# Performance work log

Measured on AMD Instinct MI355X. Metric: run time of the kernel, lower is better.

Reference implementation:

```python
import math
import jax, jax.numpy as jnp
import numpy as np

B, T, E, H = 4, 2048, 1024, 16
S = E // H
SCALE = 1.0 / math.sqrt(S)
LN_EPS = 1e-5


def setup_inputs() -> dict:
    key = jax.random.key(0)
    ks = jax.random.split(key, 5)
    w_std = 1.0 / math.sqrt(E)
    return {
        "x": jax.random.normal(ks[0], (B, T, E), jnp.float32),
        "Wq": jax.random.normal(ks[1], (E, E), jnp.float32) * w_std,
        "Wk": jax.random.normal(ks[2], (E, E), jnp.float32) * w_std,
        "Wv": jax.random.normal(ks[3], (E, E), jnp.float32) * w_std,
        "Wu": jax.random.normal(ks[4], (E, E), jnp.float32) * w_std,
        "bu": jnp.zeros((E,), jnp.float32),
        "q_gamma": jnp.ones((S,), jnp.float32),
        "q_beta": jnp.zeros((S,), jnp.float32),
        "k_gamma": jnp.ones((S,), jnp.float32),
        "k_beta": jnp.zeros((S,), jnp.float32),
    }


def _layernorm(x, gamma, beta):
    # normalize over last (head) dim, eps matches torch LayerNorm default
    mu = jnp.mean(x, axis=-1, keepdims=True)
    var = jnp.mean(jnp.square(x - mu), axis=-1, keepdims=True)
    return (x - mu) * jax.lax.rsqrt(var + LN_EPS) * gamma + beta


def reference(x, Wq, Wk, Wv, Wu, bu, q_gamma, q_beta, k_gamma, k_beta):
    b, t, e = x.shape
    h, s = H, S
    # torch Linear: y = x @ W^T ; split into heads [b, t, h, s]
    q = (x @ Wq.T).reshape(b, t, h, s)
    k = (x @ Wk.T).reshape(b, t, h, s)
    v = (x @ Wv.T).reshape(b, t, h, s)
    # kqnorm: LayerNorm over head dim s
    q = _layernorm(q, q_gamma, q_beta)
    k = _layernorm(k, k_gamma, k_beta)
    # scaled dot-product scores [b, h, t, t]
    dots = jnp.einsum("bthd,bThd->bhtT", q, k) * SCALE
    causal = jnp.tril(jnp.ones((t, t), dtype=bool))
    dots = jnp.where(causal, dots, jnp.finfo(dots.dtype).min)
    attn = jax.nn.softmax(dots, axis=-1)
    out = jnp.einsum("bhtT,bThd->bthd", attn, v).reshape(b, t, e)
    return out @ Wu.T + bu
```

## Files before the change

kernel.cpp:

```cpp
#include <hip/hip_runtime.h>
#include <hip/hip_bf16.h>
#include <stdint.h>
#include <stddef.h>


using bf16 = __hip_bfloat16;
typedef __attribute__((ext_vector_type(8))) short s16x8;
typedef __attribute__((ext_vector_type(4))) short s16x4;
typedef __attribute__((ext_vector_type(4))) float f32x4;

#define MFMA16(a, b, c) __builtin_amdgcn_mfma_f32_16x16x32_bf16((a), (b), (c), 0, 0, 0)

static __device__ __forceinline__ s16x8 ld8(const bf16* p) {
    return *reinterpret_cast<const s16x8*>(p);
}
static __device__ __forceinline__ s16x8 ld8s(const short* p) {
    return *reinterpret_cast<const s16x8*>(p);
}
static __device__ __forceinline__ s16x8 cvt8(const float* p) {
    f32x4 u = *reinterpret_cast<const f32x4*>(p);
    f32x4 v = *reinterpret_cast<const f32x4*>(p + 4);
    s16x8 r;
#pragma unroll
    for (int e = 0; e < 4; e++) {
        r[e]     = __builtin_bit_cast(short, __float2bfloat16(u[e]));
        r[e + 4] = __builtin_bit_cast(short, __float2bfloat16(v[e]));
    }
    return r;
}

static __device__ __forceinline__ void async16(short* lds, const bf16* g) {
    __builtin_amdgcn_global_load_lds(
        (const __attribute__((address_space(1))) unsigned int*)g,
        (__attribute__((address_space(3))) unsigned int*)lds, 16, 0, 0);
}

#define EE 1024

__global__ __launch_bounds__(256) void cvt_all(
    const float* __restrict__ w0, const float* __restrict__ w1,
    const float* __restrict__ w2, const float* __restrict__ w3,
    const float* __restrict__ x,
    bf16* __restrict__ o0, bf16* __restrict__ o1,
    bf16* __restrict__ o2, bf16* __restrict__ o3, bf16* __restrict__ xb)
{
    const int z = blockIdx.z;
    const float* s;
    bf16* d;
    if (z < 4) {
        s = (z == 0) ? w0 : (z == 1) ? w1 : (z == 2) ? w2 : w3;
        d = (z == 0) ? o0 : (z == 1) ? o1 : (z == 2) ? o2 : o3;
    } else {
        s = x  + (size_t)(z - 4) * 1048576;
        d = xb + (size_t)(z - 4) * 1048576;
    }
    size_t i = ((size_t)blockIdx.x * 256 + threadIdx.x) * 8;
    *reinterpret_cast<s16x8*>(d + i) = cvt8(s + i);
}

template <int AF32>
__global__ __launch_bounds__(256) void gemm_qkv_t(
    const float* __restrict__ xf, const bf16* __restrict__ xb,
    const bf16* __restrict__ Wq, const bf16* __restrict__ Wk, const bf16* __restrict__ Wv,
    bf16* __restrict__ Qb, bf16* __restrict__ Kb, bf16* __restrict__ Vb,
    const float* __restrict__ qg, const float* __restrict__ qbt,
    const float* __restrict__ kg, const float* __restrict__ kbt)
{
    constexpr int SA = AF32 ? 40 : 32;
    const int z = blockIdx.z;
    const bf16* Bt = (z == 0) ? Wq : (z == 1) ? Wk : Wv;
    bf16* out      = (z == 0) ? Qb : (z == 1) ? Kb : Vb;
    const float* gamma = (z == 0) ? qg : kg;
    const float* beta  = (z == 0) ? qbt : kbt;
    const bool  ln     = (z < 2);
    const float oscale = (z == 0) ? 0.125f : 1.0f;

    __shared__ __align__(16) short lA[128 * SA];
    __shared__ __align__(16) short lB[128 * 32];

    const int tid  = threadIdx.x;
    const int lane = tid & 63;
    const int w    = tid >> 6;
    const int wr = w >> 1, wc = w & 1;
    const int lr = lane & 15, quad = lane >> 4;

    const int m0 = blockIdx.y * 128;
    const int n0 = blockIdx.x * 128;

    const int strow = w * 32 + (lane >> 2);
    const int stcol = (lane & 3) * 8;
    const bf16* bgl = Bt + (size_t)(n0 + strow) * EE + stcol;
    short* bl = lB + (w * 2) * 512;

    const bf16* agl = nullptr;
    const float* ap = nullptr;
    short* al = lA + (w * 2) * 512;
    short* lap = nullptr;
    if constexpr (AF32) {
        const int sr  = tid >> 1;
        const int sc0 = (tid & 1) << 4;
        ap  = xf + (size_t)(m0 + sr) * EE + sc0;
        lap = lA + sr * SA + sc0;
    } else {
        agl = xb + (size_t)(m0 + strow) * EE + stcol;
    }

    f32x4 acc[4][4];
#pragma unroll
    for (int i = 0; i < 4; i++)
#pragma unroll
        for (int j = 0; j < 4; j++) acc[i][j] = (f32x4){0.f, 0.f, 0.f, 0.f};

    const short* lArd = lA + (wr * 64 + lr) * SA + quad * 8;
    const short* lBrd = lB + (wc * 64 + lr) * 32 + quad * 8;

    for (int kt = 0; kt < EE / 32; ++kt) {
        if constexpr (AF32) {
            s16x8 a0 = cvt8(ap), a1 = cvt8(ap + 8);
            __syncthreads();
            *reinterpret_cast<s16x8*>(lap)     = a0;
            *reinterpret_cast<s16x8*>(lap + 8) = a1;
            async16(bl, bgl);
            async16(bl + 512, bgl + 16 * EE);
            ap += 32;
        } else {
            __syncthreads();
            async16(al, agl);
            async16(al + 512, agl + 16 * EE);
            async16(bl, bgl);
            async16(bl + 512, bgl + 16 * EE);
            agl += 32;
        }
        bgl += 32;
        __syncthreads();

        s16x8 af[4], bfr[4];
#pragma unroll
        for (int i = 0; i < 4; i++) af[i]  = ld8s(lArd + i * 16 * SA);
#pragma unroll
        for (int j = 0; j < 4; j++) bfr[j] = ld8s(lBrd + j * 16 * 32);
#pragma unroll
        for (int i = 0; i < 4; i++)
#pragma unroll
            for (int j = 0; j < 4; j++) acc[i][j] = MFMA16(af[i], bfr[j], acc[i][j]);
    }

    if (ln) {
        float g[4], bt[4];
#pragma unroll
        for (int j = 0; j < 4; j++) {
            g[j]  = gamma[j * 16 + lr];
            bt[j] = beta[j * 16 + lr];
        }
#pragma unroll
        for (int i = 0; i < 4; i++) {
#pragma unroll
            for (int r = 0; r < 4; r++) {
                float s1 = 0.f, s2 = 0.f;
#pragma unroll
                for (int j = 0; j < 4; j++) {
                    float v = acc[i][j][r];
                    s1 += v;
                    s2 += v * v;
                }
#pragma unroll
                for (int off = 1; off < 16; off <<= 1) {
                    s1 += __shfl_xor(s1, off);
                    s2 += __shfl_xor(s2, off);
                }
                float mu  = s1 * (1.f / 64.f);
                float var = s2 * (1.f / 64.f) - mu * mu;
                float rs  = rsqrtf(var + 1e-5f);
                int row = m0 + wr * 64 + i * 16 + quad * 4 + r;
#pragma unroll
                for (int j = 0; j < 4; j++) {
                    float v = ((acc[i][j][r] - mu) * rs * g[j] + bt[j]) * oscale;
                    out[(size_t)row * EE + n0 + wc * 64 + j * 16 + lr] = __float2bfloat16(v);
                }
            }
        }
    } else {
#pragma unroll
        for (int i = 0; i < 4; i++)
#pragma unroll
            for (int r = 0; r < 4; r++) {
                int row = m0 + wr * 64 + i * 16 + quad * 4 + r;
#pragma unroll
                for (int j = 0; j < 4; j++)
                    out[(size_t)row * EE + n0 + wc * 64 + j * 16 + lr] =
                        __float2bfloat16(acc[i][j][r]);
            }
    }
}

__global__ __launch_bounds__(512, 4) void flash(
    const bf16* __restrict__ Qb, const bf16* __restrict__ Kb,
    const bf16* __restrict__ Vb, bf16* __restrict__ Ob)
{
    const int flat = blockIdx.y * 8 + blockIdx.x;
    const int vid  = (flat & 7) * 64 + (flat >> 3);
    const int pr = vid & 7;
    const int bh = vid >> 3;
    const int b = bh >> 4, h = bh & 15;
    const int tid = threadIdx.x, lane = tid & 63, w = tid >> 6;
    const int lr = lane & 15, quad = lane >> 4;
    const size_t base = (size_t)b * 2048 * 1024 + h * 64;
    const float C  = 1.44269504088896340736f;
    const float M0 = 12.0f;

    __shared__ __align__(16) short VT[64 * 72];
    __shared__ __align__(16) short PT[128 * 72];
    __shared__ __align__(16) short KS[2][64 * 64];

    short* const prow = PT + (w * 16 + lr) * 72;
    const bf16* const kst = Kb + base + (size_t)(w * 8 + (lane >> 3)) * 1024 +
                            (((lane & 7) ^ (lane >> 3)) << 3);
    short* const kdst = &KS[0][0] + w * 512;
    const int kaddr0 = lr * 64 + ((quad ^ (lr & 7)) << 3);

#pragma unroll 1
    for (int ph = 0; ph < 2; ++ph) {
        const int qt = ph ? (15 - pr) : pr;
        const int tw = qt * 128 + w * 16;

        s16x8 qf[2];
#pragma unroll
        for (int ks = 0; ks < 2; ks++)
            qf[ks] = ld8(Qb + base + (size_t)(tw + lr) * 1024 + ks * 32 + quad * 8);

        f32x4 o[4];
#pragma unroll
        for (int j = 0; j < 4; j++) o[j] = (f32x4){0.f, 0.f, 0.f, 0.f};
        float lsum = 0.f;

        const int nkt = 2 * qt + 2;

        __syncthreads();
        s16x8 va0 = ld8(Vb + base + (size_t)lane * 1024 + w * 8);
        s16x8 vb0;
        async16(kdst, kst);

#define FTILE(KT, V0C, KCUR, V0N, KNXT)                                          \
    {                                                                            \
        const int kb = (KT) * 64;                                                \
        const bool active = (kb <= tw + 15);                                     \
        __syncthreads();   \
        _Pragma("unroll")                                                        \
        for (int e = 0; e < 8; e++)                                              \
            VT[(w * 8 + e) * 72 + lane] = V0C[e];                                \
        const int kb2 = kb + 64;                                                 \
        if (kb2 < nkt * 64) {        \
            async16(kdst + (KNXT) * 4096, kst + (size_t)kb2 * 1024);             \
            V0N = ld8(Vb + base + (size_t)(kb2 + lane) * 1024 + w * 8);          \
        }                                                                        \
        if (active) {                                                            \
            const short* kc = &KS[KCUR][0];                                      \
            f32x4 sc[4];                                                         \
            _Pragma("unroll")                                                    \
            for (int jk = 0; jk < 4; jk++) sc[jk] = (f32x4){0.f, 0.f, 0.f, 0.f}; \
            _Pragma("unroll")                                                    \
            for (int ks = 0; ks < 2; ks++)                                       \
                _Pragma("unroll")                                                \
                for (int jk = 0; jk < 4; jk++) {                                 \
                    s16x8 kf = ld8s(kc + jk * 1024 + (kaddr0 ^ (ks * 32)));      \
                    sc[jk] = MFMA16(kf, qf[ks], sc[jk]);                         \
                }                                                                \
            const bool needmask = (kb + 63 > tw);                                \
            const int qq = tw + lr;                                              \
            _Pragma("unroll")                                                    \
            for (int jk = 0; jk < 4; jk++) {                                     \
                s16x4 pk;                                                        \
                _Pragma("unroll")                                                \
                for (int r = 0; r < 4; r++) {                                    \
                    float p = exp2f(fmaf(sc[jk][r], C, -M0));                    \
                    if (needmask && (kb + jk * 16 + quad * 4 + r > qq))          \
                        p = 0.f;                                                 \
                    lsum += p;                                                   \
                    pk[r] = __builtin_bit_cast(short, __float2bfloat16(p));      \
                }                                                                \
                *reinterpret_cast<s16x4*>(prow + jk * 16 + quad * 4) = pk;       \
            }                                                                    \
        }                                                                        \
        __syncthreads();                                      \
        if (active) {                                                            \
            _Pragma("unroll")                                                    \
            for (int ks = 0; ks < 2; ks++) {                                     \
                s16x8 pf = ld8s(prow + ks * 32 + quad * 8);                      \
                s16x8 vf[4];                                                     \
                _Pragma("unroll")                                                \
                for (int j = 0; j < 4; j++)                                      \
                    vf[j] = ld8s(VT + (j * 16 + lr) * 72 + ks * 32 + quad * 8);  \
                _Pragma("unroll")                                                \
                for (int j = 0; j < 4; j++)                                      \
                    o[j] = MFMA16(pf, vf[j], o[j]);                              \
            }                                                                    \
        }                                                                        \
    }

#pragma unroll 1
        for (int kt = 0; kt < nkt; kt += 2) {
            FTILE(kt,     va0, 0, vb0, 1)
            FTILE(kt + 1, vb0, 1, va0, 0)
        }
#undef FTILE

        float l = lsum;
        l += __shfl_xor(l, 16);
        l += __shfl_xor(l, 32);
#pragma unroll
        for (int r = 0; r < 4; r++) {
            float inv = 1.f / __shfl(l, quad * 4 + r);
            int t = tw + quad * 4 + r;
#pragma unroll
            for (int j = 0; j < 4; j++)
                Ob[base + (size_t)t * 1024 + j * 16 + lr] =
                    __float2bfloat16(o[j][r] * inv);
        }
    }
}

__global__ __launch_bounds__(256) void gemm_bias(
    const bf16* __restrict__ A, const bf16* __restrict__ Bt,
    const float* __restrict__ bias, float* __restrict__ out)
{
    __shared__ __align__(16) short lA[128 * 32];
    __shared__ __align__(16) short lB[128 * 32];

    const int tid  = threadIdx.x;
    const int lane = tid & 63;
    const int w    = tid >> 6;
    const int wr = w >> 1, wc = w & 1;
    const int lr = lane & 15, quad = lane >> 4;

    const int m0 = blockIdx.y * 128;
    const int n0 = blockIdx.x * 128;

    const int strow = w * 32 + (lane >> 2);
    const int stcol = (lane & 3) * 8;
    const bf16* agl = A  + (size_t)(m0 + strow) * EE + stcol;
    const bf16* bgl = Bt + (size_t)(n0 + strow) * EE + stcol;
    short* al = lA + (w * 2) * 512;
    short* bl = lB + (w * 2) * 512;

    f32x4 acc[4][4];
#pragma unroll
    for (int i = 0; i < 4; i++)
#pragma unroll
        for (int j = 0; j < 4; j++) acc[i][j] = (f32x4){0.f, 0.f, 0.f, 0.f};

    const short* lArd = lA + (wr * 64 + lr) * 32 + quad * 8;
    const short* lBrd = lB + (wc * 64 + lr) * 32 + quad * 8;

    for (int kt = 0; kt < EE / 32; ++kt) {
        __syncthreads();
        async16(al, agl);
        async16(al + 512, agl + 16 * EE);
        async16(bl, bgl);
        async16(bl + 512, bgl + 16 * EE);
        agl += 32;
        bgl += 32;
        __syncthreads();

        s16x8 af[4], bfr[4];
#pragma unroll
        for (int i = 0; i < 4; i++) af[i]  = ld8s(lArd + i * 16 * 32);
#pragma unroll
        for (int j = 0; j < 4; j++) bfr[j] = ld8s(lBrd + j * 16 * 32);
#pragma unroll
        for (int i = 0; i < 4; i++)
#pragma unroll
            for (int j = 0; j < 4; j++) acc[i][j] = MFMA16(af[i], bfr[j], acc[i][j]);
    }

    float bz[4];
#pragma unroll
    for (int j = 0; j < 4; j++)
        bz[j] = bias[n0 + wc * 64 + j * 16 + lr];
#pragma unroll
    for (int i = 0; i < 4; i++)
#pragma unroll
        for (int r = 0; r < 4; r++) {
            int row = m0 + wr * 64 + i * 16 + quad * 4 + r;
#pragma unroll
            for (int j = 0; j < 4; j++)
                out[(size_t)row * EE + n0 + wc * 64 + j * 16 + lr] =
                    acc[i][j][r] + bz[j];
        }
}

extern "C" void kernel_launch(void* const* d_in, const int* in_sizes, int n_in,
                              void* d_out, int out_size, void* d_ws, size_t ws_size,
                              hipStream_t stream)
{
    (void)in_sizes; (void)n_in; (void)out_size;
    const float* x   = (const float*)d_in[0];
    const float* Wq  = (const float*)d_in[1];
    const float* Wk  = (const float*)d_in[2];
    const float* Wv  = (const float*)d_in[3];
    const float* Wu  = (const float*)d_in[4];
    const float* bu  = (const float*)d_in[5];
    const float* qg  = (const float*)d_in[6];
    const float* qbt = (const float*)d_in[7];
    const float* kg  = (const float*)d_in[8];
    const float* kbt = (const float*)d_in[9];
    float* out = (float*)d_out;

    bf16* Qb  = (bf16*)d_ws;
    bf16* Kb  = Qb  + (size_t)8192 * 1024;
    bf16* Vb  = Kb  + (size_t)8192 * 1024;
    bf16* Wqb = Vb  + (size_t)8192 * 1024;
    bf16* Wkb = Wqb + (size_t)1024 * 1024;
    bf16* Wvb = Wkb + (size_t)1024 * 1024;
    bf16* Wub = Wvb + (size_t)1024 * 1024;
    bf16* xb  = Wub + (size_t)1024 * 1024;

    const size_t need = ((size_t)3 * 8192 * 1024 + 4 * 1024 * 1024 + 8192 * 1024) * 2;
    const bool fast = ws_size >= need;

    cvt_all<<<dim3(512, 1, fast ? 12 : 4), 256, 0, stream>>>(
        Wq, Wk, Wv, Wu, x, Wqb, Wkb, Wvb, Wub, xb);
    if (fast)
        gemm_qkv_t<0><<<dim3(8, 64, 3), 256, 0, stream>>>(
            x, xb, Wqb, Wkb, Wvb, Qb, Kb, Vb, qg, qbt, kg, kbt);
    else
        gemm_qkv_t<1><<<dim3(8, 64, 3), 256, 0, stream>>>(
            x, nullptr, Wqb, Wkb, Wvb, Qb, Kb, Vb, qg, qbt, kg, kbt);
    flash<<<dim3(8, 64), 512, 0, stream>>>(Qb, Kb, Vb, Qb);
    gemm_bias<<<dim3(8, 64), 256, 0, stream>>>(Qb, Wub, bu, out);
}
```

Measured before the change: 296.4 us.

## Double-buffer LDS loads in bf16 GEMMs and remap blocks for grouped tile order

The bf16-input QKV projection and the output projection GEMM now keep two LDS stages. The loads for the next k-tile are issued before the MFMAs of the current tile, and explicit vmcnt/lgkmcnt waits with raw barriers replace the two __syncthreads per iteration. The block-to-tile mapping is also remapped so groups of 8 M-tiles share an N-tile, which should improve L2 reuse. This doubles LDS use per block, which may lower occupancy, and it relies on hand-written wait counts being correct.

```diff
diff --git a/kernel.cpp b/kernel.cpp
--- a/kernel.cpp
+++ b/kernel.cpp
@@ -66,7 +66,6 @@
     const float* __restrict__ qg, const float* __restrict__ qbt,
     const float* __restrict__ kg, const float* __restrict__ kbt)
 {
-    constexpr int SA = AF32 ? 40 : 32;
     const int z = blockIdx.z;
     const bf16* Bt = (z == 0) ? Wq : (z == 1) ? Wk : Wv;
     bf16* out      = (z == 0) ? Qb : (z == 1) ? Kb : Vb;
@@ -75,8 +74,9 @@
     const bool  ln     = (z < 2);
     const float oscale = (z == 0) ? 0.125f : 1.0f;
 
-    __shared__ __align__(16) short lA[128 * SA];
-    __shared__ __align__(16) short lB[128 * 32];
+    constexpr int LASZ = AF32 ? 128 * 40 : 2 * 4096;
+    __shared__ __align__(16) short lA[LASZ];
+    __shared__ __align__(16) short lB[2 * 4096];
 
     const int tid  = threadIdx.x;
     const int lane = tid & 63;
@@ -84,65 +84,97 @@
     const int wr = w >> 1, wc = w & 1;
     const int lr = lane & 15, quad = lane >> 4;
 
-    const int m0 = blockIdx.y * 128;
-    const int n0 = blockIdx.x * 128;
+    const int mi = blockIdx.x * 8 + (blockIdx.y & 7);
+    const int ni = blockIdx.y >> 3;
+    const int m0 = mi * 128;
+    const int n0 = ni * 128;
 
     const int strow = w * 32 + (lane >> 2);
     const int stcol = (lane & 3) * 8;
     const bf16* bgl = Bt + (size_t)(n0 + strow) * EE + stcol;
-    short* bl = lB + (w * 2) * 512;
-
-    const bf16* agl = nullptr;
-    const float* ap = nullptr;
-    short* al = lA + (w * 2) * 512;
-    short* lap = nullptr;
+
+    f32x4 acc[4][4];
+#pragma unroll
+    for (int i = 0; i < 4; i++)
+#pragma unroll
+        for (int j = 0; j < 4; j++) acc[i][j] = (f32x4){0.f, 0.f, 0.f, 0.f};
+
     if constexpr (AF32) {
+        constexpr int SA = 40;
         const int sr  = tid >> 1;
         const int sc0 = (tid & 1) << 4;
-        ap  = xf + (size_t)(m0 + sr) * EE + sc0;
-        lap = lA + sr * SA + sc0;
-    } else {
-        agl = xb + (size_t)(m0 + strow) * EE + stcol;
-    }
-
-    f32x4 acc[4][4];
-#pragma unroll
-    for (int i = 0; i < 4; i++)
-#pragma unroll
-        for (int j = 0; j < 4; j++) acc[i][j] = (f32x4){0.f, 0.f, 0.f, 0.f};
-
-    const short* lArd = lA + (wr * 64 + lr) * SA + quad * 8;
-    const short* lBrd = lB + (wc * 64 + lr) * 32 + quad * 8;
-
-    for (int kt = 0; kt < EE / 32; ++kt) {
-        if constexpr (AF32) {
+        const float* ap = xf + (size_t)(m0 + sr) * EE + sc0;
+        short* lap = lA + sr * SA + sc0;
+        short* bl = lB + (w * 2) * 512;
+        const short* lArd = lA + (wr * 64 + lr) * SA + quad * 8;
+        const short* lBrd = lB + (wc * 64 + lr) * 32 + quad * 8;
+        const bf16* bg = bgl;
+
+        for (int kt = 0; kt < EE / 32; ++kt) {
             s16x8 a0 = cvt8(ap), a1 = cvt8(ap + 8);
             __syncthreads();
             *reinterpret_cast<s16x8*>(lap)     = a0;
             *reinterpret_cast<s16x8*>(lap + 8) = a1;
-            async16(bl, bgl);
-            async16(bl + 512, bgl + 16 * EE);
+            async16(bl, bg);
+            async16(bl + 512, bg + 16 * EE);
             ap += 32;
-        } else {
+            bg += 32;
             __syncthreads();
-            async16(al, agl);
-            async16(al + 512, agl + 16 * EE);
-            async16(bl, bgl);
-            async16(bl + 512, bgl + 16 * EE);
-            agl += 32;
-        }
-        bgl += 32;
-        __syncthreads();
-
-        s16x8 af[4], bfr[4];
-#pragma unroll
-        for (int i = 0; i < 4; i++) af[i]  = ld8s(lArd + i * 16 * SA);
-#pragma unroll
-        for (int j = 0; j < 4; j++) bfr[j] = ld8s(lBrd + j * 16 * 32);
-#pragma unroll
-        for (int i = 0; i < 4; i++)
-#pragma unroll
-            for (int j = 0; j < 4; j++) acc[i][j] = MFMA16(af[i], bfr[j], acc[i][j]);
+
+            s16x8 af[4], bfr[4];
+#pragma unroll
+            for (int i = 0; i < 4; i++) af[i]  = ld8s(lArd + i * 16 * SA);
+#pragma unroll
+            for (int j = 0; j < 4; j++) bfr[j] = ld8s(lBrd + j * 16 * 32);
+#pragma unroll
+            for (int i = 0; i < 4; i++)
+#pragma unroll
+                for (int j = 0; j < 4; j++) acc[i][j] = MFMA16(af[i], bfr[j], acc[i][j]);
+        }
+    } else {
+        const bf16* agl = xb + (size_t)(m0 + strow) * EE + stcol;
+        short* const al0 = lA + w * 1024;
+        short* const bl0 = lB + w * 1024;
+
+#define QSTAGE(c, kt)                                                     \
+    {                                                                     \
+        short* al = al0 + (c) * 4096;                                     \
+        short* bl = bl0 + (c) * 4096;                                     \
+        const bf16* ag = agl + (kt) * 32;                                 \
+        const bf16* bg = bgl + (kt) * 32;                                 \
+        async16(al, ag); async16(al + 512, ag + 16 * EE);                 \
+        async16(bl, bg); async16(bl + 512, bg + 16 * EE);                 \
+    }
+
+        QSTAGE(0, 0)
+#pragma unroll 1
+        for (int kt = 0; kt < EE / 32; ++kt) {
+            const int c = kt & 1;
+            if (kt < EE / 32 - 1) {
+                QSTAGE(c ^ 1, kt + 1)
+                asm volatile("s_waitcnt vmcnt(4)" ::: "memory");
+            } else {
+                asm volatile("s_waitcnt vmcnt(0)" ::: "memory");
+            }
+            __builtin_amdgcn_s_barrier();
+
+            const short* lArd = lA + c * 4096 + (wr * 64 + lr) * 32 + quad * 8;
+            const short* lBrd = lB + c * 4096 + (wc * 64 + lr) * 32 + quad * 8;
+            s16x8 af[4], bfr[4];
+#pragma unroll
+            for (int i = 0; i < 4; i++) af[i]  = ld8s(lArd + i * 512);
+#pragma unroll
+            for (int j = 0; j < 4; j++) bfr[j] = ld8s(lBrd + j * 512);
+            __builtin_amdgcn_sched_barrier(0);
+            asm volatile("s_waitcnt lgkmcnt(0)" ::: "memory");
+            __builtin_amdgcn_sched_barrier(0);
+#pragma unroll
+            for (int i = 0; i < 4; i++)
+#pragma unroll
+                for (int j = 0; j < 4; j++) acc[i][j] = MFMA16(af[i], bfr[j], acc[i][j]);
+            __builtin_amdgcn_s_barrier();
+        }
+#undef QSTAGE
     }
 
     if (ln) {
@@ -323,8 +355,8 @@
     const bf16* __restrict__ A, const bf16* __restrict__ Bt,
     const float* __restrict__ bias, float* __restrict__ out)
 {
-    __shared__ __align__(16) short lA[128 * 32];
-    __shared__ __align__(16) short lB[128 * 32];
+    __shared__ __align__(16) short lA[2 * 4096];
+    __shared__ __align__(16) short lB[2 * 4096];
 
     const int tid  = threadIdx.x;
     const int lane = tid & 63;
@@ -332,15 +364,17 @@
     const int wr = w >> 1, wc = w & 1;
     const int lr = lane & 15, quad = lane >> 4;
 
-    const int m0 = blockIdx.y * 128;
-    const int n0 = blockIdx.x * 128;
+    const int mi = blockIdx.x * 8 + (blockIdx.y & 7);
+    const int ni = blockIdx.y >> 3;
+    const int m0 = mi * 128;
+    const int n0 = ni * 128;
 
     const int strow = w * 32 + (lane >> 2);
     const int stcol = (lane & 3) * 8;
     const bf16* agl = A  + (size_t)(m0 + strow) * EE + stcol;
     const bf16* bgl = Bt + (size_t)(n0 + strow) * EE + stcol;
-    short* al = lA + (w * 2) * 512;
-    short* bl = lB + (w * 2) * 512;
+    short* const al0 = lA + w * 1024;
+    short* const bl0 = lB + w * 1024;
 
     f32x4 acc[4][4];
 #pragma unroll
@@ -348,29 +382,45 @@
 #pragma unroll
         for (int j = 0; j < 4; j++) acc[i][j] = (f32x4){0.f, 0.f, 0.f, 0.f};
 
-    const short* lArd = lA + (wr * 64 + lr) * 32 + quad * 8;
-    const short* lBrd = lB + (wc * 64 + lr) * 32 + quad * 8;
-
+#define BSTAGE(c, kt)                                                     \
+    {                                                                     \
+        short* al = al0 + (c) * 4096;                                     \
+        short* bl = bl0 + (c) * 4096;                                     \
+        const bf16* ag = agl + (kt) * 32;                                 \
+        const bf16* bg = bgl + (kt) * 32;                                 \
+        async16(al, ag); async16(al + 512, ag + 16 * EE);                 \
+        async16(bl, bg); async16(bl + 512, bg + 16 * EE);                 \
+    }
+
+    BSTAGE(0, 0)
+#pragma unroll 1
     for (int kt = 0; kt < EE / 32; ++kt) {
-        __syncthreads();
-        async16(al, agl);
-        async16(al + 512, agl + 16 * EE);
-        async16(bl, bgl);
-        async16(bl + 512, bgl + 16 * EE);
-        agl += 32;
-        bgl += 32;
-        __syncthreads();
-
+        const int c = kt & 1;
+        if (kt < EE / 32 - 1) {
+            BSTAGE(c ^ 1, kt + 1)
+            asm volatile("s_waitcnt vmcnt(4)" ::: "memory");
+        } else {
+            asm volatile("s_waitcnt vmcnt(0)" ::: "memory");
+        }
+        __builtin_amdgcn_s_barrier();
+
+        const short* lArd = lA + c * 4096 + (wr * 64 + lr) * 32 + quad * 8;
+        const short* lBrd = lB + c * 4096 + (wc * 64 + lr) * 32 + quad * 8;
         s16x8 af[4], bfr[4];
 #pragma unroll
-        for (int i = 0; i < 4; i++) af[i]  = ld8s(lArd + i * 16 * 32);
-#pragma unroll
-        for (int j = 0; j < 4; j++) bfr[j] = ld8s(lBrd + j * 16 * 32);
+        for (int i = 0; i < 4; i++) af[i]  = ld8s(lArd + i * 512);
+#pragma unroll
+        for (int j = 0; j < 4; j++) bfr[j] = ld8s(lBrd + j * 512);
+        __builtin_amdgcn_sched_barrier(0);
+        asm volatile("s_waitcnt lgkmcnt(0)" ::: "memory");
+        __builtin_amdgcn_sched_barrier(0);
 #pragma unroll
         for (int i = 0; i < 4; i++)
 #pragma unroll
             for (int j = 0; j < 4; j++) acc[i][j] = MFMA16(af[i], bfr[j], acc[i][j]);
-    }
+        __builtin_amdgcn_s_barrier();
+    }
+#undef BSTAGE
 
     float bz[4];
 #pragma unroll
```

Result: faster. 284.0 us (-4.2%).
